# Kernel optimization log

Hardware: AMD Instinct MI355X
Metric: run time of the kernel (lower is better)

The kernel has to match this reference:

```python
import jax, jax.numpy as jnp
import numpy as np

B, S, H, F, E, K = 4, 2048, 512, 2048, 8, 2


def setup_inputs() -> dict:
    key = jax.random.key(0)
    ks = jax.random.split(key, 6)
    s_h = 1.0 / np.sqrt(H)
    s_f = 1.0 / np.sqrt(F)
    return {
        "x": jax.random.normal(ks[0], (B, S, H), dtype=jnp.float32),
        "router_w": jax.random.uniform(ks[1], (E, H), jnp.float32, -s_h, s_h),
        "fc1_w": jax.random.uniform(ks[2], (E, F, H), jnp.float32, -s_h, s_h),
        "fc1_b": jax.random.uniform(ks[3], (E, F), jnp.float32, -s_h, s_h),
        "fc2_w": jax.random.uniform(ks[4], (E, H, F), jnp.float32, -s_f, s_f),
        "fc2_b": jax.random.uniform(ks[5], (E, H), jnp.float32, -s_f, s_f),
    }


def reference(x, router_w, fc1_w, fc1_b, fc2_w, fc2_b):
    # Router: Linear (no bias), softmax over experts, top-k, renormalize.
    logits = jnp.einsum("bsh,eh->bse", x, router_w)           # [B,S,E]
    probs = jax.nn.softmax(logits, axis=-1)                    # [B,S,E]
    topk_p, topk_i = jax.lax.top_k(probs, K)                   # [B,S,K]
    topk_p = topk_p / (jnp.sum(topk_p, axis=-1, keepdims=True) + 1e-9)

    # Original loop runs every expert FFN on all tokens and masks;
    # mathematically identical: dense per-expert FFN, then gather+combine.
    h1 = jnp.einsum("bsh,efh->bsef", x, fc1_w) + fc1_b         # [B,S,E,F]
    a = jax.nn.gelu(h1, approximate=False)                     # exact erf GELU (torch nn.GELU default)
    y = jnp.einsum("bsef,ehf->bseh", a, fc2_w) + fc2_b         # [B,S,E,H]

    sel = jnp.take_along_axis(y, topk_i[..., None], axis=2)    # [B,S,K,H]
    output = jnp.sum(topk_p[..., None] * sel, axis=2)          # [B,S,H]
    return output, probs, topk_i
```

## Files before the change

kernel.cpp:

```cpp
#include <hip/hip_runtime.h>

#define T_TOKENS 8192
#define HD 512
#define FD 2048
#define NE 8
#define CAP 8192
#define CSTRIDE 32

typedef __attribute__((ext_vector_type(8))) short short8;
typedef __attribute__((ext_vector_type(4))) float f32x4;

__device__ __forceinline__ ushort f2bf(float f) {
  union { float f; unsigned u; } v; v.f = f;
  unsigned u = v.u;
  return (ushort)((u + 0x7fffu + ((u >> 16) & 1u)) >> 16);
}

__device__ __forceinline__ void gld16(const ushort* g, ushort* l) {
  __builtin_amdgcn_global_load_lds(
      (const __attribute__((address_space(1))) void*)g,
      (__attribute__((address_space(3))) void*)l, 16, 0, 0);
}

__global__ void cvt_bf16(const float4* __restrict__ src, ushort4* __restrict__ dst, int n4) {
  int i = blockIdx.x * blockDim.x + threadIdx.x;
  int st = gridDim.x * blockDim.x;
  for (; i < n4; i += st) {
    float4 v = src[i];
    ushort4 o;
    o.x = f2bf(v.x); o.y = f2bf(v.y); o.z = f2bf(v.z); o.w = f2bf(v.w);
    dst[i] = o;
  }
}

#define TPW 16
__global__ void router_kernel(const float* __restrict__ x, const float* __restrict__ rw,
                              float* __restrict__ probs_out, float* __restrict__ topk_out,
                              int* __restrict__ counts, int* __restrict__ bucket_tok,
                              float* __restrict__ bucket_w, int4* __restrict__ tok_info) {
  __shared__ int lcnt[NE];
  __shared__ int lbase[NE];
  __shared__ int ls_e0[64], ls_e1[64], ls_s0[64], ls_s1[64];
  __shared__ float ls_w0[64], ls_w1[64];

  int wave = threadIdx.x >> 6, lane = threadIdx.x & 63;
  if (threadIdx.x < NE) lcnt[threadIdx.x] = 0;
  __syncthreads();

  int tbase = blockIdx.x * 64;
  for (int it = 0; it < TPW; it++) {
    int lt = wave * TPW + it;
    int t = tbase + lt;
    float acc[NE];
#pragma unroll
    for (int e = 0; e < NE; e++) acc[e] = 0.f;
    const float* xr = x + (size_t)t * HD;
    for (int c = 0; c < HD; c += 64) {
      float xv = xr[c + lane];
#pragma unroll
      for (int e = 0; e < NE; e++) acc[e] += xv * rw[e * HD + c + lane];
    }
#pragma unroll
    for (int e = 0; e < NE; e++) {
#pragma unroll
      for (int s = 32; s > 0; s >>= 1) acc[e] += __shfl_xor(acc[e], s, 64);
    }
    if (lane == 0) {
      float m = acc[0];
#pragma unroll
      for (int e = 1; e < NE; e++) m = fmaxf(m, acc[e]);
      float p[NE], s = 0.f;
#pragma unroll
      for (int e = 0; e < NE; e++) { p[e] = expf(acc[e] - m); s += p[e]; }
      float inv = 1.f / s;
#pragma unroll
      for (int e = 0; e < NE; e++) { p[e] *= inv; probs_out[(size_t)t * NE + e] = p[e]; }
      int i0 = 0;
#pragma unroll
      for (int e = 1; e < NE; e++) if (p[e] > p[i0]) i0 = e;
      int i1 = (i0 == 0) ? 1 : 0;
#pragma unroll
      for (int e = 0; e < NE; e++) if (e != i0 && p[e] > p[i1]) i1 = e;
      float r = 1.f / (p[i0] + p[i1] + 1e-9f);
      topk_out[(size_t)t * 2 + 0] = (float)i0;
      topk_out[(size_t)t * 2 + 1] = (float)i1;
      ls_e0[lt] = i0; ls_e1[lt] = i1;
      ls_w0[lt] = p[i0] * r; ls_w1[lt] = p[i1] * r;
      ls_s0[lt] = atomicAdd(&lcnt[i0], 1);
      ls_s1[lt] = atomicAdd(&lcnt[i1], 1);
    }
  }
  __syncthreads();
  if (threadIdx.x < NE)
    lbase[threadIdx.x] = atomicAdd(&counts[threadIdx.x * CSTRIDE], lcnt[threadIdx.x]);
  __syncthreads();
  if (threadIdx.x < 64) {
    int lt = threadIdx.x, t = tbase + lt;
    int e0 = ls_e0[lt], e1 = ls_e1[lt];
    int g0 = lbase[e0] + ls_s0[lt];
    int g1 = lbase[e1] + ls_s1[lt];
    bucket_tok[e0 * CAP + g0] = t; bucket_w[e0 * CAP + g0] = ls_w0[lt];
    bucket_tok[e1 * CAP + g1] = t; bucket_w[e1 * CAP + g1] = ls_w1[lt];
    tok_info[t] = make_int4(e0, e1, g0, g1);
  }
}

__global__ void scan_kernel(const int* __restrict__ counts, int* __restrict__ offsets) {
  if (threadIdx.x == 0) {
    int o = 0;
#pragma unroll
    for (int e = 0; e < NE; e++) { offsets[e] = o; o += counts[e * CSTRIDE]; }
  }
}


__device__ __forceinline__ short8 ldsr(const ushort* base, int row, int ks, int q) {
  int a = row * 128 + ks * 64 + q * 16;
  a ^= (row & 7) << 4;
  return *(const short8*)((const char*)base + a);
}

template <bool IS_FC1>
__global__ __launch_bounds__(256, 2)
void ffn_gemm_db(const ushort* __restrict__ Ab, const ushort* __restrict__ Bw,
                 const float* __restrict__ bias, const int* __restrict__ counts,
                 const int* __restrict__ offsets, const int* __restrict__ bucket_tok,
                 const float* __restrict__ bucket_w, ushort* __restrict__ Aout,
                 float* __restrict__ Yout, int KD, int ND) {
  constexpr int ATILE = 128 * 64;

  int e = blockIdx.z;
  int cnt = counts[e * CSTRIDE];
  int m0 = blockIdx.y * 128;
  if (m0 >= cnt) return;
  int n0 = blockIdx.x * 128;
  int off = offsets[e];

  extern __shared__ ushort smem[];
  ushort* ldsA = smem;
  ushort* ldsB = smem + 2 * ATILE;

  int tid = threadIdx.x;
  int lid = tid & 63, w = tid >> 6;
  int wm = w >> 1, wn = w & 1;
  int q = lid >> 4, l16 = lid & 15;
  int r0 = tid >> 3;
  int colElem = (((tid & 7) ^ (r0 & 7)) << 3);

  const ushort *aS[4], *bS[4];
#pragma unroll
  for (int u = 0; u < 4; ++u) {
    int rA = min(m0 + u * 32 + r0, cnt - 1);
    int tok = IS_FC1 ? bucket_tok[e * CAP + rA] : (off + rA);
    aS[u] = Ab + (size_t)tok * KD + colElem;
    bS[u] = Bw + ((size_t)e * ND + n0 + u * 32 + r0) * KD + colElem;
  }

  f32x4 acc[4][4] = {};
  int nk = KD >> 6;

  auto STG = [&](int kt) {
    ushort* la = ldsA + ((kt & 1) ? ATILE : 0) + tid * 8;
    ushort* lb = ldsB + ((kt & 1) ? ATILE : 0) + tid * 8;
#pragma unroll
    for (int u = 0; u < 4; ++u) {
      gld16(aS[u] + kt * 64, la + u * 2048);
      gld16(bS[u] + kt * 64, lb + u * 2048);
    }
  };

  STG(0);
  __syncthreads();

  for (int kt = 0; kt < nk; ++kt) {
    if (kt + 1 < nk) STG(kt + 1);
    const ushort* As = ldsA + ((kt & 1) ? ATILE : 0);
    const ushort* Bs = ldsB + ((kt & 1) ? ATILE : 0);
    short8 af[4][2], bfr[4][2];
#pragma unroll
    for (int mi = 0; mi < 4; ++mi)
#pragma unroll
      for (int ks = 0; ks < 2; ++ks)
        af[mi][ks] = ldsr(As, wm * 64 + mi * 16 + l16, ks, q);
#pragma unroll
    for (int nj = 0; nj < 4; ++nj)
#pragma unroll
      for (int ks = 0; ks < 2; ++ks)
        bfr[nj][ks] = ldsr(Bs, wn * 64 + nj * 16 + l16, ks, q);
#pragma unroll
    for (int mi = 0; mi < 4; ++mi)
#pragma unroll
      for (int nj = 0; nj < 4; ++nj)
#pragma unroll
        for (int ks = 0; ks < 2; ++ks)
          acc[mi][nj] = __builtin_amdgcn_mfma_f32_16x16x32_bf16(
              af[mi][ks], bfr[nj][ks], acc[mi][nj], 0, 0, 0);
    __syncthreads();
  }

  float bcol[4];
#pragma unroll
  for (int j = 0; j < 4; ++j)
    bcol[j] = bias[(size_t)e * ND + n0 + wn * 64 + j * 16 + l16];

  if (IS_FC1) {
    ushort* Ct = smem;
#pragma unroll
    for (int i = 0; i < 4; i++) {
      __syncthreads();
#pragma unroll
      for (int j = 0; j < 4; j++)
#pragma unroll
        for (int r = 0; r < 4; r++) {
          float v = acc[i][j][r] + bcol[j];
          float g = 0.5f * v * (1.0f + erff(v * 0.70710678118654752f));
          Ct[(wm * 16 + q * 4 + r) * 136 + wn * 64 + j * 16 + l16] = f2bf(g);
        }
      __syncthreads();
#pragma unroll
      for (int u = 0; u < 2; u++) {
        int c = tid + u * 256;
        int ml = c >> 4, cc = c & 15;
        int gm = m0 + (ml >> 4) * 64 + i * 16 + (ml & 15);
        if (gm < cnt)
          *(uint4*)&Aout[(size_t)(off + gm) * ND + n0 + cc * 8] =
              *(const uint4*)&Ct[ml * 136 + cc * 8];
      }
    }
  } else {
    float* Cf = (float*)smem;
#pragma unroll
    for (int i = 0; i < 4; i++) {
      __syncthreads();
#pragma unroll
      for (int r = 0; r < 4; r++) {
        int gm = m0 + wm * 64 + i * 16 + q * 4 + r;
        float wgt = bucket_w[e * CAP + min(gm, cnt - 1)];
#pragma unroll
        for (int j = 0; j < 4; j++)
          Cf[(wm * 16 + q * 4 + r) * 132 + wn * 64 + j * 16 + l16] = wgt * (acc[i][j][r] + bcol[j]);
      }
      __syncthreads();
#pragma unroll
      for (int u = 0; u < 4; u++) {
        int c = tid + u * 256;
        int ml = c >> 5, cc = c & 31;
        int gm = m0 + (ml >> 4) * 64 + i * 16 + (ml & 15);
        if (gm < cnt)
          *(float4*)&Yout[(size_t)(off + gm) * ND + n0 + cc * 4] =
              *(const float4*)&Cf[ml * 132 + cc * 4];
      }
    }
  }
}

__global__ void combine_kernel(const float4* __restrict__ Y, const int4* __restrict__ tok_info,
                               const int* __restrict__ offsets, float4* __restrict__ out) {
  int t = blockIdx.x;
  int4 ti = tok_info[t];
  int g0 = offsets[ti.x] + ti.z;
  int g1 = offsets[ti.y] + ti.w;
  int i = threadIdx.x;
  float4 a = Y[(size_t)g0 * (HD / 4) + i];
  float4 b = Y[(size_t)g1 * (HD / 4) + i];
  out[(size_t)t * (HD / 4) + i] = make_float4(a.x + b.x, a.y + b.y, a.z + b.z, a.w + b.w);
}

extern "C" void kernel_launch(void* const* d_in, const int* in_sizes, int n_in,
                              void* d_out, int out_size, void* d_ws, size_t ws_size,
                              hipStream_t stream) {
  const float* x    = (const float*)d_in[0];
  const float* rw   = (const float*)d_in[1];
  const float* fc1w = (const float*)d_in[2];
  const float* fc1b = (const float*)d_in[3];
  const float* fc2w = (const float*)d_in[4];
  const float* fc2b = (const float*)d_in[5];

  float* out   = (float*)d_out;
  float* probs = out + (size_t)T_TOKENS * HD;
  float* topk  = probs + (size_t)T_TOKENS * NE;

  static bool attr_done = false;
  if (!attr_done) {
    (void)hipFuncSetAttribute((const void*)&ffn_gemm_db<true>,
                              hipFuncAttributeMaxDynamicSharedMemorySize, 65536);
    (void)hipFuncSetAttribute((const void*)&ffn_gemm_db<false>,
                              hipFuncAttributeMaxDynamicSharedMemorySize, 65536);
    attr_done = true;
  }

  char* p = (char*)d_ws;
  auto carve = [&](size_t bytes) { char* r = p; p += (bytes + 255) & ~(size_t)255; return r; };
  int*    counts     = (int*)carve(NE * CSTRIDE * sizeof(int));
  int*    offsets    = (int*)carve(NE * sizeof(int));
  int*    bucket_tok = (int*)carve((size_t)NE * CAP * sizeof(int));
  float*  bucket_w   = (float*)carve((size_t)NE * CAP * sizeof(float));
  int4*   tok_info   = (int4*)carve((size_t)T_TOKENS * sizeof(int4));
  ushort* xb   = (ushort*)carve((size_t)T_TOKENS * HD * 2);
  ushort* w1b  = (ushort*)carve((size_t)NE * FD * HD * 2);
  ushort* w2b  = (ushort*)carve((size_t)NE * HD * FD * 2);
  ushort* Abuf = (ushort*)carve((size_t)T_TOKENS * 2 * FD * 2);
  float*  Y    = (float*)carve((size_t)T_TOKENS * 2 * HD * 4);

  hipMemsetAsync(counts, 0, NE * CSTRIDE * sizeof(int), stream);
  cvt_bf16<<<2048, 256, 0, stream>>>((const float4*)x, (ushort4*)xb, T_TOKENS * HD / 4);
  cvt_bf16<<<2048, 256, 0, stream>>>((const float4*)fc1w, (ushort4*)w1b, NE * FD * HD / 4);
  cvt_bf16<<<2048, 256, 0, stream>>>((const float4*)fc2w, (ushort4*)w2b, NE * HD * FD / 4);
  router_kernel<<<T_TOKENS / 64, 256, 0, stream>>>(x, rw, probs, topk, counts, bucket_tok,
                                                   bucket_w, tok_info);
  scan_kernel<<<1, 64, 0, stream>>>(counts, offsets);

  ffn_gemm_db<true><<<dim3(FD / 128, CAP / 128, NE), 256, 65536, stream>>>(
      xb, w1b, fc1b, counts, offsets, bucket_tok, bucket_w, Abuf, nullptr, HD, FD);
  ffn_gemm_db<false><<<dim3(HD / 128, CAP / 128, NE), 256, 65536, stream>>>(
      Abuf, w2b, fc2b, counts, offsets, bucket_tok, bucket_w, nullptr, Y, FD, HD);

  combine_kernel<<<T_TOKENS, 128, 0, stream>>>((const float4*)Y, tok_info, offsets, (float4*)out);
}
```

Measured before the change: 334.2 us.

## Use triple-buffered K=32 GEMM pipeline with explicit waits and fuse bf16 conversions

The expert GEMM drops from a double-buffered K=64 tile to a triple-buffered K=32 tile. It uses explicit vmcnt waits, sched barriers and setprio around the MFMA block, and adjusts the LDS swizzle for the 64-byte rows. Shared memory per block falls to 48KB and launch bounds ask for 3 blocks per CU, aiming to overlap global loads with compute and raise occupancy. The three fp32-to-bf16 conversion launches are merged into one kernel to save launch overhead. The risks are more barriers per K step and register pressure at the higher occupancy target.

```diff
diff --git a/kernel.cpp b/kernel.cpp
--- a/kernel.cpp
+++ b/kernel.cpp
@@ -22,14 +22,21 @@
       (__attribute__((address_space(3))) void*)l, 16, 0, 0);
 }
 
-__global__ void cvt_bf16(const float4* __restrict__ src, ushort4* __restrict__ dst, int n4) {
+__global__ void cvt_bf16_3(const float4* __restrict__ s0, ushort4* __restrict__ d0, int c0,
+                           const float4* __restrict__ s1, ushort4* __restrict__ d1, int c1,
+                           const float4* __restrict__ s2, ushort4* __restrict__ d2, int c2) {
   int i = blockIdx.x * blockDim.x + threadIdx.x;
   int st = gridDim.x * blockDim.x;
-  for (; i < n4; i += st) {
-    float4 v = src[i];
+  int nt = c0 + c1 + c2;
+  for (; i < nt; i += st) {
+    const float4* s; ushort4* d; int j = i;
+    if (j < c0) { s = s0; d = d0; }
+    else if ((j -= c0) < c1) { s = s1; d = d1; }
+    else { j -= c1; s = s2; d = d2; }
+    float4 v = s[j];
     ushort4 o;
     o.x = f2bf(v.x); o.y = f2bf(v.y); o.z = f2bf(v.z); o.w = f2bf(v.w);
-    dst[i] = o;
+    d[j] = o;
   }
 }
 
@@ -114,20 +121,46 @@
 }
 
 
-__device__ __forceinline__ short8 ldsr(const ushort* base, int row, int ks, int q) {
-  int a = row * 128 + ks * 64 + q * 16;
-  a ^= (row & 7) << 4;
+__device__ __forceinline__ short8 ldsr32(const ushort* base, int row, int q) {
+  int a = row * 64 + q * 16;
+  a ^= ((row >> 1) & 3) << 4;
   return *(const short8*)((const char*)base + a);
 }
 
+#define VMC(N) asm volatile("s_waitcnt vmcnt(" #N ")" ::: "memory")
+#define SB0 __builtin_amdgcn_sched_barrier(0)
+
+#define STG3(KT, SB_) do { \
+    ushort* _la = bufA + (SB_) * TU + tid * 8; \
+    ushort* _lb = bufB + (SB_) * TU + tid * 8; \
+    gld16(aS0 + (KT) * 32, _la); gld16(aS1 + (KT) * 32, _la + 2048); \
+    gld16(bS0 + (KT) * 32, _lb); gld16(bS1 + (KT) * 32, _lb + 2048); \
+  } while (0)
+
+#define CMP3(RB_) do { \
+    const ushort* _As = bufA + (RB_) * TU; \
+    const ushort* _Bs = bufB + (RB_) * TU; \
+    short8 af[4], bfr[4]; \
+    _Pragma("unroll") for (int mi = 0; mi < 4; ++mi) \
+      af[mi] = ldsr32(_As, wm * 64 + mi * 16 + l16, q); \
+    _Pragma("unroll") for (int nj = 0; nj < 4; ++nj) \
+      bfr[nj] = ldsr32(_Bs, wn * 64 + nj * 16 + l16, q); \
+    asm volatile("s_waitcnt lgkmcnt(0)" ::: "memory"); SB0; \
+    __builtin_amdgcn_s_setprio(1); \
+    _Pragma("unroll") for (int mi = 0; mi < 4; ++mi) \
+      _Pragma("unroll") for (int nj = 0; nj < 4; ++nj) \
+        acc[mi][nj] = __builtin_amdgcn_mfma_f32_16x16x32_bf16(af[mi], bfr[nj], acc[mi][nj], 0, 0, 0); \
+    __builtin_amdgcn_s_setprio(0); \
+  } while (0)
+
 template <bool IS_FC1>
-__global__ __launch_bounds__(256, 2)
-void ffn_gemm_db(const ushort* __restrict__ Ab, const ushort* __restrict__ Bw,
+__global__ __launch_bounds__(256, 3)
+void ffn_gemm_p3(const ushort* __restrict__ Ab, const ushort* __restrict__ Bw,
                  const float* __restrict__ bias, const int* __restrict__ counts,
                  const int* __restrict__ offsets, const int* __restrict__ bucket_tok,
                  const float* __restrict__ bucket_w, ushort* __restrict__ Aout,
                  float* __restrict__ Yout, int KD, int ND) {
-  constexpr int ATILE = 128 * 64;
+  constexpr int TU = 128 * 32;
 
   int e = blockIdx.z;
   int cnt = counts[e * CSTRIDE];
@@ -137,66 +170,47 @@
   int off = offsets[e];
 
   extern __shared__ ushort smem[];
-  ushort* ldsA = smem;
-  ushort* ldsB = smem + 2 * ATILE;
+  ushort* bufA = smem;
+  ushort* bufB = smem + 3 * TU;
 
   int tid = threadIdx.x;
   int lid = tid & 63, w = tid >> 6;
   int wm = w >> 1, wn = w & 1;
   int q = lid >> 4, l16 = lid & 15;
-  int r0 = tid >> 3;
-  int colElem = (((tid & 7) ^ (r0 & 7)) << 3);
-
-  const ushort *aS[4], *bS[4];
-#pragma unroll
-  for (int u = 0; u < 4; ++u) {
-    int rA = min(m0 + u * 32 + r0, cnt - 1);
-    int tok = IS_FC1 ? bucket_tok[e * CAP + rA] : (off + rA);
-    aS[u] = Ab + (size_t)tok * KD + colElem;
-    bS[u] = Bw + ((size_t)e * ND + n0 + u * 32 + r0) * KD + colElem;
+  int r0 = tid >> 2;
+  int colElem = (((tid & 3) ^ ((r0 >> 1) & 3)) << 3);
+
+  const ushort *aS0, *aS1, *bS0, *bS1;
+  {
+    int rA0 = min(m0 + r0, cnt - 1);
+    int rA1 = min(m0 + 64 + r0, cnt - 1);
+    int t0 = IS_FC1 ? bucket_tok[e * CAP + rA0] : (off + rA0);
+    int t1 = IS_FC1 ? bucket_tok[e * CAP + rA1] : (off + rA1);
+    aS0 = Ab + (size_t)t0 * KD + colElem;
+    aS1 = Ab + (size_t)t1 * KD + colElem;
+    bS0 = Bw + ((size_t)e * ND + n0 + r0) * KD + colElem;
+    bS1 = Bw + ((size_t)e * ND + n0 + 64 + r0) * KD + colElem;
   }
 
   f32x4 acc[4][4] = {};
-  int nk = KD >> 6;
-
-  auto STG = [&](int kt) {
-    ushort* la = ldsA + ((kt & 1) ? ATILE : 0) + tid * 8;
-    ushort* lb = ldsB + ((kt & 1) ? ATILE : 0) + tid * 8;
-#pragma unroll
-    for (int u = 0; u < 4; ++u) {
-      gld16(aS[u] + kt * 64, la + u * 2048);
-      gld16(bS[u] + kt * 64, lb + u * 2048);
-    }
-  };
-
-  STG(0);
-  __syncthreads();
-
-  for (int kt = 0; kt < nk; ++kt) {
-    if (kt + 1 < nk) STG(kt + 1);
-    const ushort* As = ldsA + ((kt & 1) ? ATILE : 0);
-    const ushort* Bs = ldsB + ((kt & 1) ? ATILE : 0);
-    short8 af[4][2], bfr[4][2];
-#pragma unroll
-    for (int mi = 0; mi < 4; ++mi)
-#pragma unroll
-      for (int ks = 0; ks < 2; ++ks)
-        af[mi][ks] = ldsr(As, wm * 64 + mi * 16 + l16, ks, q);
-#pragma unroll
-    for (int nj = 0; nj < 4; ++nj)
-#pragma unroll
-      for (int ks = 0; ks < 2; ++ks)
-        bfr[nj][ks] = ldsr(Bs, wn * 64 + nj * 16 + l16, ks, q);
-#pragma unroll
-    for (int mi = 0; mi < 4; ++mi)
-#pragma unroll
-      for (int nj = 0; nj < 4; ++nj)
-#pragma unroll
-        for (int ks = 0; ks < 2; ++ks)
-          acc[mi][nj] = __builtin_amdgcn_mfma_f32_16x16x32_bf16(
-              af[mi][ks], bfr[nj][ks], acc[mi][nj], 0, 0, 0);
-    __syncthreads();
-  }
+  int nk = KD >> 5;
+
+  STG3(0, 0); STG3(1, 1);
+  int rb = 0, sb = 2;
+  for (int k = 0; k < nk - 2; ++k) {
+    STG3(k + 2, sb); SB0;
+    VMC(8); SB0;
+    __builtin_amdgcn_s_barrier(); SB0;
+    CMP3(rb);
+    SB0; __builtin_amdgcn_s_barrier();
+    rb = (rb == 2) ? 0 : rb + 1;
+    sb = (sb == 2) ? 0 : sb + 1;
+  }
+  VMC(4); SB0; __builtin_amdgcn_s_barrier(); SB0;
+  CMP3(rb); SB0; __builtin_amdgcn_s_barrier();
+  rb = (rb == 2) ? 0 : rb + 1;
+  VMC(0); SB0; __builtin_amdgcn_s_barrier(); SB0;
+  CMP3(rb); SB0; __builtin_amdgcn_s_barrier();
 
   float bcol[4];
 #pragma unroll
@@ -282,10 +296,10 @@
 
   static bool attr_done = false;
   if (!attr_done) {
-    (void)hipFuncSetAttribute((const void*)&ffn_gemm_db<true>,
-                              hipFuncAttributeMaxDynamicSharedMemorySize, 65536);
-    (void)hipFuncSetAttribute((const void*)&ffn_gemm_db<false>,
-                              hipFuncAttributeMaxDynamicSharedMemorySize, 65536);
+    (void)hipFuncSetAttribute((const void*)&ffn_gemm_p3<true>,
+                              hipFuncAttributeMaxDynamicSharedMemorySize, 49152);
+    (void)hipFuncSetAttribute((const void*)&ffn_gemm_p3<false>,
+                              hipFuncAttributeMaxDynamicSharedMemorySize, 49152);
     attr_done = true;
   }
 
@@ -303,16 +317,17 @@
   float*  Y    = (float*)carve((size_t)T_TOKENS * 2 * HD * 4);
 
   hipMemsetAsync(counts, 0, NE * CSTRIDE * sizeof(int), stream);
-  cvt_bf16<<<2048, 256, 0, stream>>>((const float4*)x, (ushort4*)xb, T_TOKENS * HD / 4);
-  cvt_bf16<<<2048, 256, 0, stream>>>((const float4*)fc1w, (ushort4*)w1b, NE * FD * HD / 4);
-  cvt_bf16<<<2048, 256, 0, stream>>>((const float4*)fc2w, (ushort4*)w2b, NE * HD * FD / 4);
+  cvt_bf16_3<<<4096, 256, 0, stream>>>(
+      (const float4*)x,    (ushort4*)xb,  T_TOKENS * HD / 4,
+      (const float4*)fc1w, (ushort4*)w1b, NE * FD * HD / 4,
+      (const float4*)fc2w, (ushort4*)w2b, NE * HD * FD / 4);
   router_kernel<<<T_TOKENS / 64, 256, 0, stream>>>(x, rw, probs, topk, counts, bucket_tok,
                                                    bucket_w, tok_info);
   scan_kernel<<<1, 64, 0, stream>>>(counts, offsets);
 
-  ffn_gemm_db<true><<<dim3(FD / 128, CAP / 128, NE), 256, 65536, stream>>>(
+  ffn_gemm_p3<true><<<dim3(FD / 128, CAP / 128, NE), 256, 49152, stream>>>(
       xb, w1b, fc1b, counts, offsets, bucket_tok, bucket_w, Abuf, nullptr, HD, FD);
-  ffn_gemm_db<false><<<dim3(HD / 128, CAP / 128, NE), 256, 65536, stream>>>(
+  ffn_gemm_p3<false><<<dim3(HD / 128, CAP / 128, NE), 256, 49152, stream>>>(
       Abuf, w2b, fc2b, counts, offsets, bucket_tok, bucket_w, nullptr, Y, FD, HD);
 
   combine_kernel<<<T_TOKENS, 128, 0, stream>>>((const float4*)Y, tok_info, offsets, (float4*)out);
```

After: 314.3 us. 6.0% less time.
